# Performance work log

Hardware: AMD Instinct MI355X
Metric: run time of the kernel (lower is better)

## Reference

```python
import jax, jax.numpy as jnp
import numpy as np

B, S, D = 4, 2048, 1024  # batch, seq_len, model dim (= qk_dim = output_dim)


def setup_inputs() -> dict:
    key = jax.random.key(0)
    kq, kk, kv, kwq, kwk, kwv = jax.random.split(key, 6)
    q = jax.random.normal(kq, (B, S, D), dtype=jnp.float32)
    k = jax.random.normal(kk, (B, S, D), dtype=jnp.float32)
    v = jax.random.normal(kv, (B, S, D), dtype=jnp.float32)
    # causal mask, broadcast over batch
    mask = jnp.broadcast_to(jnp.tril(jnp.ones((S, S), dtype=bool)), (B, S, S))
    W_q = jax.random.uniform(kwq, (D, D), dtype=jnp.float32)
    W_k = jax.random.uniform(kwk, (D, D), dtype=jnp.float32)
    W_v = jax.random.uniform(kwv, (D, D), dtype=jnp.float32)
    return {"q": q, "k": k, "v": v, "mask": mask, "W_q": W_q, "W_k": W_k, "W_v": W_v}


def reference(q, k, v, mask, W_q, W_k, W_v):
    q1 = q @ W_q  # (B, S, D)
    k1 = k @ W_k  # (B, S, D)
    v1 = v @ W_v  # (B, S, D)
    qk = jnp.einsum('bij,bkj->bik', q1, k1)  # (B, S, S)
    qk = qk * jax.lax.rsqrt(float(k1.shape[-1]))
    neg_inf = jnp.finfo(jnp.float32).min
    qk = jnp.where(mask, qk, neg_inf)
    s = jax.nn.softmax(qk, axis=-1)
    return jnp.einsum('bij,bjk->bik', s, v1)
```

## Files before the change

kernel.cpp:

```cpp
#include <hip/hip_runtime.h>
#include <hip/hip_bf16.h>
#include <float.h>


typedef __attribute__((ext_vector_type(8))) short bf16x8;
typedef __attribute__((ext_vector_type(4))) float f32x4;

#define MFMA16 __builtin_amdgcn_mfma_f32_16x16x32_bf16

union U8 { bf16x8 v; unsigned w[4]; };

__device__ __forceinline__ ushort f2bf(float x) {
  union { float f; unsigned u; } v; v.f = x;
  unsigned r = v.u + 0x7fffu + ((v.u >> 16) & 1u);
  return (ushort)(r >> 16);
}
__device__ __forceinline__ float bf2f(ushort h) {
  union { unsigned u; float f; } v; v.u = ((unsigned)h) << 16;
  return v.f;
}
__device__ __forceinline__ void splitf(float x, ushort& hi, ushort& lo) {
  hi = f2bf(x);
  lo = f2bf(x - bf2f(hi));
}

__device__ __forceinline__ bf16x8 cvt8(const float* lp) {
  U8 H;
#pragma unroll
  for (int p = 0; p < 4; ++p) {
    const unsigned u0 = __float_as_uint(lp[2 * p]);
    const unsigned u1 = __float_as_uint(lp[2 * p + 1]);
    const unsigned r0 = (u0 + 0x7fffu + ((u0 >> 16) & 1u)) >> 16;
    const unsigned r1 = (u1 + 0x7fffu + ((u1 >> 16) & 1u)) & 0xffff0000u;
    H.w[p] = r0 | r1;
  }
  return H.v;
}

#define GLOAD16(gp, lp)                                                        \
  __builtin_amdgcn_global_load_lds(                                            \
      (const __attribute__((address_space(1))) void*)(gp),                     \
      (__attribute__((address_space(3))) void*)(lp), 16, 0, 0)

__device__ __forceinline__ void stage_bf16_32(const ushort* g, int pitch,
                                              ushort* lds, int w, int lane) {
#pragma unroll
  for (int i = 0; i < 2; ++i) {
    const int c = w * 2 + i;
    const int row = c * 16 + (lane >> 2);
    const int kp = (lane & 3) * 8;
    GLOAD16(g + (size_t)row * pitch + kp, lds + c * 512);
  }
}
__device__ __forceinline__ void stage_bf16_64(const ushort* g, int pitch,
                                              ushort* lds, int w, int lane) {
#pragma unroll
  for (int i = 0; i < 4; ++i) {
    const int c = w * 4 + i;
    const int row = c * 8 + (lane >> 3);
    const int kp = (lane & 7) * 8;
    GLOAD16(g + (size_t)row * pitch + kp, lds + c * 512);
  }
}
__device__ __forceinline__ void stage_f32_32(const float* g, int pitch,
                                             float* lds, int w, int lane) {
#pragma unroll
  for (int i = 0; i < 4; ++i) {
    const int c = w * 4 + i;
    const int row = c * 8 + (lane >> 3);
    const int kp = (lane & 7) * 4;
    GLOAD16(g + (size_t)row * pitch + kp, lds + c * 256);
  }
}

__global__ __launch_bounds__(256) void split_pre(
    const float* __restrict__ q, const float* __restrict__ k,
    ushort* __restrict__ qh, ushort* __restrict__ ql,
    ushort* __restrict__ kh, ushort* __restrict__ kl) {
  const float* X = blockIdx.y ? k : q;
  ushort* H = blockIdx.y ? kh : qh;
  ushort* L = blockIdx.y ? kl : ql;
  const int n4 = 2097152;
  for (int i = blockIdx.x * 256 + threadIdx.x; i < n4; i += 2048 * 256) {
    const float4 x = reinterpret_cast<const float4*>(X)[i];
    ushort h0, l0, h1, l1, h2, l2, h3, l3;
    splitf(x.x, h0, l0); splitf(x.y, h1, l1);
    splitf(x.z, h2, l2); splitf(x.w, h3, l3);
    reinterpret_cast<ushort4*>(H)[i] = ushort4{h0, h1, h2, h3};
    reinterpret_cast<ushort4*>(L)[i] = ushort4{l0, l1, l2, l3};
  }
}

__global__ __launch_bounds__(256) void wt_conv(
    const float* __restrict__ W0, const float* __restrict__ W1,
    const float* __restrict__ W2, ushort* __restrict__ Th0,
    ushort* __restrict__ Tl0, ushort* __restrict__ Th1,
    ushort* __restrict__ Tl1, ushort* __restrict__ Th2) {
  __shared__ float t[32][33];
  const int z = blockIdx.z;
  const float* W = z == 0 ? W0 : (z == 1 ? W1 : W2);
  ushort* Th = z == 0 ? Th0 : (z == 1 ? Th1 : Th2);
  ushort* Tl = z == 0 ? Tl0 : (z == 1 ? Tl1 : nullptr);
  const int bx = blockIdx.x, by = blockIdx.y;
  const int r = threadIdx.x >> 3, c4 = (threadIdx.x & 7) * 4;
  const float4 x =
      *reinterpret_cast<const float4*>(&W[(size_t)(bx * 32 + r) * 1024 + by * 32 + c4]);
  t[r][c4] = x.x; t[r][c4 + 1] = x.y; t[r][c4 + 2] = x.z; t[r][c4 + 3] = x.w;
  __syncthreads();
  ushort h[4], l[4];
#pragma unroll
  for (int j = 0; j < 4; ++j) splitf(t[c4 + j][r], h[j], l[j]);
  const size_t o = (size_t)(by * 32 + r) * 1024 + bx * 32 + c4;
  *reinterpret_cast<ushort4*>(&Th[o]) = ushort4{h[0], h[1], h[2], h[3]};
  if (Tl)
    *reinterpret_cast<ushort4*>(&Tl[o]) = ushort4{l[0], l[1], l[2], l[3]};
}

__global__ __launch_bounds__(256) void proj_qk(
    const ushort* __restrict__ Ah0, const ushort* __restrict__ Al0,
    const ushort* __restrict__ Ah1, const ushort* __restrict__ Al1,
    const ushort* __restrict__ Bh0, const ushort* __restrict__ Bl0,
    const ushort* __restrict__ Bh1, const ushort* __restrict__ Bl1,
    ushort* __restrict__ Oh0, ushort* __restrict__ Ol0,
    ushort* __restrict__ Oh1, ushort* __restrict__ Ol1) {
  __shared__ ushort Ahs[4096], Als[4096], Bhs[4096], Bls[4096];
  const int z = blockIdx.z;
  const ushort* Ah = z ? Ah1 : Ah0;
  const ushort* Al = z ? Al1 : Al0;
  const ushort* Bh = z ? Bh1 : Bh0;
  const ushort* Bl = z ? Bl1 : Bl0;
  ushort* Oh = z ? Oh1 : Oh0;
  ushort* Ol = z ? Ol1 : Ol0;
  const int tid = threadIdx.x, lane = tid & 63, w = tid >> 6;
  const int wr = w >> 1, wc = w & 1;
  const int lr = lane & 15, kg = lane >> 4;
  const int m0 = blockIdx.y * 128, n0 = blockIdx.x * 128;
  f32x4 acc[4][4] = {};

  for (int k0 = 0; k0 < 1024; k0 += 32) {
    stage_bf16_32(Ah + (size_t)m0 * 1024 + k0, 1024, Ahs, w, lane);
    stage_bf16_32(Al + (size_t)m0 * 1024 + k0, 1024, Als, w, lane);
    stage_bf16_32(Bh + (size_t)n0 * 1024 + k0, 1024, Bhs, w, lane);
    stage_bf16_32(Bl + (size_t)n0 * 1024 + k0, 1024, Bls, w, lane);
    __syncthreads();
    bf16x8 ah[4], al[4], bh[4], bl[4];
#pragma unroll
    for (int m = 0; m < 4; ++m) {
      ah[m] = *reinterpret_cast<bf16x8*>(&Ahs[(wr * 64 + m * 16 + lr) * 32 + kg * 8]);
      al[m] = *reinterpret_cast<bf16x8*>(&Als[(wr * 64 + m * 16 + lr) * 32 + kg * 8]);
    }
#pragma unroll
    for (int n = 0; n < 4; ++n) {
      bh[n] = *reinterpret_cast<bf16x8*>(&Bhs[(wc * 64 + n * 16 + lr) * 32 + kg * 8]);
      bl[n] = *reinterpret_cast<bf16x8*>(&Bls[(wc * 64 + n * 16 + lr) * 32 + kg * 8]);
    }
#pragma unroll
    for (int m = 0; m < 4; ++m)
#pragma unroll
      for (int n = 0; n < 4; ++n) {
        acc[m][n] = MFMA16(ah[m], bh[n], acc[m][n], 0, 0, 0);
        acc[m][n] = MFMA16(ah[m], bl[n], acc[m][n], 0, 0, 0);
        acc[m][n] = MFMA16(al[m], bh[n], acc[m][n], 0, 0, 0);
      }
    __syncthreads();
  }
#pragma unroll
  for (int m = 0; m < 4; ++m)
#pragma unroll
    for (int n = 0; n < 4; ++n)
#pragma unroll
      for (int reg = 0; reg < 4; ++reg) {
        const int gm = m0 + wr * 64 + m * 16 + kg * 4 + reg;
        const int gn = n0 + wc * 64 + n * 16 + lr;
        ushort h, l;
        splitf(acc[m][n][reg], h, l);
        Oh[(size_t)gm * 1024 + gn] = h;
        Ol[(size_t)gm * 1024 + gn] = l;
      }
}

__global__ __launch_bounds__(256) void proj_v(const ushort* __restrict__ Wvt,
                                              const float* __restrict__ V,
                                              ushort* __restrict__ v1t) {
  __shared__ ushort Ahs[4096];
  __shared__ float Bs[4096];
  const int tid = threadIdx.x, lane = tid & 63, w = tid >> 6;
  const int wr = w >> 1, wc = w & 1;
  const int lr = lane & 15, kg = lane >> 4;
  const int m0 = blockIdx.y * 128;
  const int n0 = blockIdx.x * 128;
  f32x4 acc[4][4] = {};

  for (int k0 = 0; k0 < 1024; k0 += 32) {
    stage_bf16_32(Wvt + (size_t)m0 * 1024 + k0, 1024, Ahs, w, lane);
    stage_f32_32(V + (size_t)n0 * 1024 + k0, 1024, Bs, w, lane);
    __syncthreads();
    bf16x8 ah[4], bh[4];
#pragma unroll
    for (int m = 0; m < 4; ++m)
      ah[m] = *reinterpret_cast<bf16x8*>(&Ahs[(wr * 64 + m * 16 + lr) * 32 + kg * 8]);
#pragma unroll
    for (int n = 0; n < 4; ++n)
      bh[n] = cvt8(&Bs[(wc * 64 + n * 16 + lr) * 32 + kg * 8]);
#pragma unroll
    for (int m = 0; m < 4; ++m)
#pragma unroll
      for (int n = 0; n < 4; ++n)
        acc[m][n] = MFMA16(ah[m], bh[n], acc[m][n], 0, 0, 0);
    __syncthreads();
  }
#pragma unroll
  for (int m = 0; m < 4; ++m)
#pragma unroll
    for (int n = 0; n < 4; ++n)
#pragma unroll
      for (int reg = 0; reg < 4; ++reg) {
        const int gm = m0 + wr * 64 + m * 16 + kg * 4 + reg;
        const int gn = n0 + wc * 64 + n * 16 + lr;
        const int b = gn >> 11, jj = gn & 2047;
        v1t[((size_t)b << 21) + (size_t)gm * 2048 + jj] = f2bf(acc[m][n][reg]);
      }
}

__global__ __launch_bounds__(256) void qk2(
    const ushort* __restrict__ q1h, const ushort* __restrict__ q1l,
    const ushort* __restrict__ k1h, const ushort* __restrict__ k1l,
    float* __restrict__ scores) {
  __shared__ ushort Ahs[4096], Als[4096], Bhs[4096], Bls[4096];
  const int tid = threadIdx.x, lane = tid & 63, w = tid >> 6;
  const int wr = w >> 1, wc = w & 1;
  const int lr = lane & 15, kg = lane >> 4;
  const int b = blockIdx.y;
  int p = blockIdx.x, ti = 0, accp = 0;
  while (accp + ti + 1 <= p) { accp += ti + 1; ++ti; }
  const int tj = p - accp;
  const ushort* qh = q1h + ((size_t)b * 2048 + ti * 128) * 1024;
  const ushort* ql = q1l + ((size_t)b * 2048 + ti * 128) * 1024;
  const ushort* kh = k1h + ((size_t)b * 2048 + tj * 128) * 1024;
  const ushort* kl = k1l + ((size_t)b * 2048 + tj * 128) * 1024;
  f32x4 acc[4][4] = {};

  for (int k0 = 0; k0 < 1024; k0 += 32) {
    stage_bf16_32(qh + k0, 1024, Ahs, w, lane);
    stage_bf16_32(ql + k0, 1024, Als, w, lane);
    stage_bf16_32(kh + k0, 1024, Bhs, w, lane);
    stage_bf16_32(kl + k0, 1024, Bls, w, lane);
    __syncthreads();
    bf16x8 ah[4], al[4], bh[4], bl[4];
#pragma unroll
    for (int m = 0; m < 4; ++m) {
      ah[m] = *reinterpret_cast<bf16x8*>(&Ahs[(wr * 64 + m * 16 + lr) * 32 + kg * 8]);
      al[m] = *reinterpret_cast<bf16x8*>(&Als[(wr * 64 + m * 16 + lr) * 32 + kg * 8]);
    }
#pragma unroll
    for (int n = 0; n < 4; ++n) {
      bh[n] = *reinterpret_cast<bf16x8*>(&Bhs[(wc * 64 + n * 16 + lr) * 32 + kg * 8]);
      bl[n] = *reinterpret_cast<bf16x8*>(&Bls[(wc * 64 + n * 16 + lr) * 32 + kg * 8]);
    }
#pragma unroll
    for (int m = 0; m < 4; ++m)
#pragma unroll
      for (int n = 0; n < 4; ++n) {
        acc[m][n] = MFMA16(ah[m], bh[n], acc[m][n], 0, 0, 0);
        acc[m][n] = MFMA16(ah[m], bl[n], acc[m][n], 0, 0, 0);
        acc[m][n] = MFMA16(al[m], bh[n], acc[m][n], 0, 0, 0);
      }
    __syncthreads();
  }
  const float sc = 0.03125f;
  float* st = scores + ((size_t)b * 136 + p) * 16384;
  const bool diag = (ti == tj);
#pragma unroll
  for (int m = 0; m < 4; ++m)
#pragma unroll
    for (int n = 0; n < 4; ++n)
#pragma unroll
      for (int reg = 0; reg < 4; ++reg) {
        const int il = wr * 64 + m * 16 + kg * 4 + reg;
        const int jl = wc * 64 + n * 16 + lr;
        float v = acc[m][n][reg] * sc;
        if (diag && jl > il) v = -FLT_MAX;
        st[il * 128 + jl] = v;
      }
}

__global__ __launch_bounds__(256) void softmax_kernel(float* __restrict__ scores) {
  __shared__ float red[8];
  const int rb = blockIdx.x;
  const int b = rb >> 11, r = rb & 2047;
  const int ti = r >> 7, rl = r & 127, ncol = (ti + 1) * 128;
  const int valid = r + 1;
  float* srow = scores + ((size_t)b * 136 + (ti * (ti + 1)) / 2) * 16384;
  const int tid = threadIdx.x, lane = tid & 63, w = tid >> 6;

  float vals[8];
  float mx = -FLT_MAX;
#pragma unroll
  for (int c = 0; c < 8; ++c) {
    const int j = tid + c * 256;
    vals[c] = (j < valid)
                  ? srow[(size_t)(j >> 7) * 16384 + rl * 128 + (j & 127)]
                  : -FLT_MAX;
    mx = fmaxf(mx, vals[c]);
  }
#pragma unroll
  for (int o = 32; o; o >>= 1) mx = fmaxf(mx, __shfl_xor(mx, o));
  if (lane == 0) red[w] = mx;
  __syncthreads();
  mx = fmaxf(fmaxf(red[0], red[1]), fmaxf(red[2], red[3]));

  float ex[8];
  float sum = 0.f;
#pragma unroll
  for (int c = 0; c < 8; ++c) {
    const int j = tid + c * 256;
    ex[c] = (j < valid) ? __expf(vals[c] - mx) : 0.f;
    sum += ex[c];
  }
#pragma unroll
  for (int o = 32; o; o >>= 1) sum += __shfl_xor(sum, o);
  if (lane == 0) red[4 + w] = sum;
  __syncthreads();
  sum = red[4] + red[5] + red[6] + red[7];
  const float inv = 1.f / sum;
#pragma unroll
  for (int c = 0; c < 8; ++c) {
    const int j = tid + c * 256;
    if (j < ncol) {
      ushort* pt = reinterpret_cast<ushort*>(srow + (size_t)(j >> 7) * 16384);
      pt[rl * 256 + (j & 127)] = f2bf(ex[c] * inv);
    }
  }
}

__global__ __launch_bounds__(256) void pv2(const float* __restrict__ scores,
                                           const ushort* __restrict__ v1t,
                                           float* __restrict__ out) {
  __shared__ ushort Ps[128 * 64], Vs[128 * 64];
  const int tid = threadIdx.x, lane = tid & 63, w = tid >> 6;
  const int wr = w >> 1, wc = w & 1;
  const int lr = lane & 15, kg = lane >> 4;
  const int b = blockIdx.z;
  const int ti = 15 - blockIdx.y;
  const int n0 = blockIdx.x * 128;
  const int tri_ti = (ti * (ti + 1)) / 2;
  const ushort* vbase = v1t + ((size_t)b << 21) + (size_t)n0 * 2048;
  const int kend = (ti + 1) * 128;
  f32x4 acc[4][4] = {};

  for (int k0 = 0; k0 < kend; k0 += 64) {
    const ushort* pt = reinterpret_cast<const ushort*>(
        scores + ((size_t)b * 136 + tri_ti + (k0 >> 7)) * 16384);
    stage_bf16_64(pt + (k0 & 64), 256, Ps, w, lane);
    stage_bf16_64(vbase + k0, 2048, Vs, w, lane);
    __syncthreads();
#pragma unroll
    for (int t2 = 0; t2 < 2; ++t2) {
      bf16x8 pa[4], vb[4];
#pragma unroll
      for (int m = 0; m < 4; ++m)
        pa[m] = *reinterpret_cast<bf16x8*>(
            &Ps[(wr * 64 + m * 16 + lr) * 64 + t2 * 32 + kg * 8]);
#pragma unroll
      for (int n = 0; n < 4; ++n)
        vb[n] = *reinterpret_cast<bf16x8*>(
            &Vs[(wc * 64 + n * 16 + lr) * 64 + t2 * 32 + kg * 8]);
#pragma unroll
      for (int m = 0; m < 4; ++m)
#pragma unroll
        for (int n = 0; n < 4; ++n)
          acc[m][n] = MFMA16(pa[m], vb[n], acc[m][n], 0, 0, 0);
    }
    __syncthreads();
  }
#pragma unroll
  for (int m = 0; m < 4; ++m)
#pragma unroll
    for (int n = 0; n < 4; ++n)
#pragma unroll
      for (int reg = 0; reg < 4; ++reg) {
        const int gm = ti * 128 + wr * 64 + m * 16 + kg * 4 + reg;
        const int gn = n0 + wc * 64 + n * 16 + lr;
        out[((size_t)b * 2048 + gm) * 1024 + gn] = acc[m][n][reg];
      }
}

extern "C" void kernel_launch(void* const* d_in, const int* in_sizes, int n_in,
                              void* d_out, int out_size, void* d_ws,
                              size_t ws_size, hipStream_t stream) {
  const float* q = (const float*)d_in[0];
  const float* k = (const float*)d_in[1];
  const float* v = (const float*)d_in[2];
  const float* Wq = (const float*)d_in[4];
  const float* Wk = (const float*)d_in[5];
  const float* Wv = (const float*)d_in[6];
  float* out = (float*)d_out;

  char* ws = (char*)d_ws;
  float* scores = (float*)ws;
  ushort* qsh = (ushort*)ws;
  ushort* qsl = qsh + 8388608;
  ushort* ksh = qsh + 2 * 8388608;
  ushort* ksl = qsh + 3 * 8388608;
  ushort* v1t = (ushort*)(ws + 37748736);
  ushort* q1hi = (ushort*)(ws + 67108864);
  ushort* q1lo = q1hi + 8388608;
  ushort* k1hi = q1hi + 2 * 8388608;
  ushort* k1lo = q1hi + 3 * 8388608;
  ushort* Wqth = (ushort*)(ws + 134217728);
  ushort* Wqtl = Wqth + 1048576;
  ushort* Wkth = Wqth + 2097152;
  ushort* Wktl = Wqth + 3145728;
  ushort* Wvt  = Wqth + 4194304;
  const size_t need = 134217728 + 10485760;
  if (ws_size < need) return;

  dim3 blk(256);
  wt_conv<<<dim3(32, 32, 3), blk, 0, stream>>>(Wq, Wk, Wv, Wqth, Wqtl, Wkth,
                                               Wktl, Wvt);
  split_pre<<<dim3(2048, 2), blk, 0, stream>>>(q, k, qsh, qsl, ksh, ksl);
  proj_qk<<<dim3(8, 64, 2), blk, 0, stream>>>(qsh, qsl, ksh, ksl, Wqth, Wqtl,
                                              Wkth, Wktl, q1hi, q1lo, k1hi,
                                              k1lo);
  proj_v<<<dim3(64, 8), blk, 0, stream>>>(Wvt, v, v1t);
  qk2<<<dim3(136, 4), blk, 0, stream>>>(q1hi, q1lo, k1hi, k1lo, scores);
  softmax_kernel<<<dim3(8192), blk, 0, stream>>>(scores);
  pv2<<<dim3(8, 16, 4), blk, 0, stream>>>(scores, v1t, out);
}
```

Baseline: 359.8 us.

## Split QK^T reduction dimension across two blocks and sum partials in softmax

The QK score kernel now splits the 1024-long reduction into two halves along a new grid z dimension, writing two partial score buffers that the softmax kernel adds when loading. This doubles the block count for the 544-block QK launch to improve CU occupancy on the wide GPU. The cost is an extra scores buffer write and read, and a larger workspace. The diagonal masking moves entirely into the softmax's valid-column check, and proj_v is reordered after softmax so v1t can reuse the q1 region.

```diff
diff --git a/kernel.cpp b/kernel.cpp
--- a/kernel.cpp
+++ b/kernel.cpp
@@ -225,22 +225,23 @@
 __global__ __launch_bounds__(256) void qk2(
     const ushort* __restrict__ q1h, const ushort* __restrict__ q1l,
     const ushort* __restrict__ k1h, const ushort* __restrict__ k1l,
-    float* __restrict__ scores) {
+    float* __restrict__ scoresA, float* __restrict__ scoresB) {
   __shared__ ushort Ahs[4096], Als[4096], Bhs[4096], Bls[4096];
   const int tid = threadIdx.x, lane = tid & 63, w = tid >> 6;
   const int wr = w >> 1, wc = w & 1;
   const int lr = lane & 15, kg = lane >> 4;
   const int b = blockIdx.y;
+  const int kh0 = blockIdx.z * 512;
   int p = blockIdx.x, ti = 0, accp = 0;
   while (accp + ti + 1 <= p) { accp += ti + 1; ++ti; }
   const int tj = p - accp;
-  const ushort* qh = q1h + ((size_t)b * 2048 + ti * 128) * 1024;
-  const ushort* ql = q1l + ((size_t)b * 2048 + ti * 128) * 1024;
-  const ushort* kh = k1h + ((size_t)b * 2048 + tj * 128) * 1024;
-  const ushort* kl = k1l + ((size_t)b * 2048 + tj * 128) * 1024;
+  const ushort* qh = q1h + ((size_t)b * 2048 + ti * 128) * 1024 + kh0;
+  const ushort* ql = q1l + ((size_t)b * 2048 + ti * 128) * 1024 + kh0;
+  const ushort* kh = k1h + ((size_t)b * 2048 + tj * 128) * 1024 + kh0;
+  const ushort* kl = k1l + ((size_t)b * 2048 + tj * 128) * 1024 + kh0;
   f32x4 acc[4][4] = {};
 
-  for (int k0 = 0; k0 < 1024; k0 += 32) {
+  for (int k0 = 0; k0 < 512; k0 += 32) {
     stage_bf16_32(qh + k0, 1024, Ahs, w, lane);
     stage_bf16_32(ql + k0, 1024, Als, w, lane);
     stage_bf16_32(kh + k0, 1024, Bhs, w, lane);
@@ -268,8 +269,7 @@
     __syncthreads();
   }
   const float sc = 0.03125f;
-  float* st = scores + ((size_t)b * 136 + p) * 16384;
-  const bool diag = (ti == tj);
+  float* st = (blockIdx.z ? scoresB : scoresA) + ((size_t)b * 136 + p) * 16384;
 #pragma unroll
   for (int m = 0; m < 4; ++m)
 #pragma unroll
@@ -278,19 +278,20 @@
       for (int reg = 0; reg < 4; ++reg) {
         const int il = wr * 64 + m * 16 + kg * 4 + reg;
         const int jl = wc * 64 + n * 16 + lr;
-        float v = acc[m][n][reg] * sc;
-        if (diag && jl > il) v = -FLT_MAX;
-        st[il * 128 + jl] = v;
-      }
-}
-
-__global__ __launch_bounds__(256) void softmax_kernel(float* __restrict__ scores) {
+        st[il * 128 + jl] = acc[m][n][reg] * sc;
+      }
+}
+
+__global__ __launch_bounds__(256) void softmax_kernel(
+    float* __restrict__ scoresA, const float* __restrict__ scoresB) {
   __shared__ float red[8];
   const int rb = blockIdx.x;
   const int b = rb >> 11, r = rb & 2047;
   const int ti = r >> 7, rl = r & 127, ncol = (ti + 1) * 128;
   const int valid = r + 1;
-  float* srow = scores + ((size_t)b * 136 + (ti * (ti + 1)) / 2) * 16384;
+  const size_t tbase = ((size_t)b * 136 + (ti * (ti + 1)) / 2) * 16384;
+  float* srowA = scoresA + tbase;
+  const float* srowB = scoresB + tbase;
   const int tid = threadIdx.x, lane = tid & 63, w = tid >> 6;
 
   float vals[8];
@@ -298,9 +299,8 @@
 #pragma unroll
   for (int c = 0; c < 8; ++c) {
     const int j = tid + c * 256;
-    vals[c] = (j < valid)
-                  ? srow[(size_t)(j >> 7) * 16384 + rl * 128 + (j & 127)]
-                  : -FLT_MAX;
+    const size_t o = (size_t)(j >> 7) * 16384 + rl * 128 + (j & 127);
+    vals[c] = (j < valid) ? (srowA[o] + srowB[o]) : -FLT_MAX;
     mx = fmaxf(mx, vals[c]);
   }
 #pragma unroll
@@ -327,7 +327,7 @@
   for (int c = 0; c < 8; ++c) {
     const int j = tid + c * 256;
     if (j < ncol) {
-      ushort* pt = reinterpret_cast<ushort*>(srow + (size_t)(j >> 7) * 16384);
+      ushort* pt = reinterpret_cast<ushort*>(srowA + (size_t)(j >> 7) * 16384);
       pt[rl * 256 + (j & 127)] = f2bf(ex[c] * inv);
     }
   }
@@ -397,22 +397,24 @@
   float* out = (float*)d_out;
 
   char* ws = (char*)d_ws;
-  float* scores = (float*)ws;
+  const size_t SCORES_T = 35651584;
+  float* scoresA = (float*)ws;
+  float* scoresB = (float*)(ws + SCORES_T);
   ushort* qsh = (ushort*)ws;
   ushort* qsl = qsh + 8388608;
   ushort* ksh = qsh + 2 * 8388608;
   ushort* ksl = qsh + 3 * 8388608;
-  ushort* v1t = (ushort*)(ws + 37748736);
-  ushort* q1hi = (ushort*)(ws + 67108864);
+  ushort* q1hi = (ushort*)(ws + 2 * SCORES_T);
   ushort* q1lo = q1hi + 8388608;
   ushort* k1hi = q1hi + 2 * 8388608;
   ushort* k1lo = q1hi + 3 * 8388608;
-  ushort* Wqth = (ushort*)(ws + 134217728);
+  ushort* v1t = (ushort*)(ws + 2 * SCORES_T);
+  ushort* Wqth = (ushort*)(ws + 2 * SCORES_T + 67108864);
   ushort* Wqtl = Wqth + 1048576;
   ushort* Wkth = Wqth + 2097152;
   ushort* Wktl = Wqth + 3145728;
   ushort* Wvt  = Wqth + 4194304;
-  const size_t need = 134217728 + 10485760;
+  const size_t need = 2 * SCORES_T + 67108864 + 10485760;
   if (ws_size < need) return;
 
   dim3 blk(256);
@@ -422,8 +424,9 @@
   proj_qk<<<dim3(8, 64, 2), blk, 0, stream>>>(qsh, qsl, ksh, ksl, Wqth, Wqtl,
                                               Wkth, Wktl, q1hi, q1lo, k1hi,
                                               k1lo);
+  qk2<<<dim3(136, 4, 2), blk, 0, stream>>>(q1hi, q1lo, k1hi, k1lo, scoresA,
+                                           scoresB);
+  softmax_kernel<<<dim3(8192), blk, 0, stream>>>(scoresA, scoresB);
   proj_v<<<dim3(64, 8), blk, 0, stream>>>(Wvt, v, v1t);
-  qk2<<<dim3(136, 4), blk, 0, stream>>>(q1hi, q1lo, k1hi, k1lo, scores);
-  softmax_kernel<<<dim3(8192), blk, 0, stream>>>(scores);
-  pv2<<<dim3(8, 16, 4), blk, 0, stream>>>(scores, v1t, out);
-}
+  pv2<<<dim3(8, 16, 4), blk, 0, stream>>>(scoresA, v1t, out);
+}
```

New measurement: 350.6 us. 2.6% less time.
